# Optimization experiments

Hardware: AMD Instinct MI355X
Metric: run time of the kernel (lower is better)

Reference implementation:

```python
import jax, jax.numpy as jnp
import numpy as np

N = 50000
E = 800000
IN_CH = 256
HEADS = 4
OUT_CH = 32
NEG_SLOPE = 0.2
EPS = 1e-16


def setup_inputs() -> dict:
    key = jax.random.key(0)
    k1, k2, k3, k4 = jax.random.split(key, 4)
    x = jax.random.normal(k1, (N, IN_CH), dtype=jnp.float32)
    edge_index = jax.random.randint(k2, (2, E), 0, N, dtype=jnp.int32)
    # xavier-ish scaling for stability
    weight = jax.random.normal(k3, (HEADS, IN_CH, OUT_CH), dtype=jnp.float32) * (1.0 / np.sqrt(IN_CH))
    att = jax.random.normal(k4, (HEADS, 2 * OUT_CH), dtype=jnp.float32) * (1.0 / np.sqrt(2 * OUT_CH))
    bias = jnp.zeros((HEADS * OUT_CH,), dtype=jnp.float32)
    return {"x": x, "edge_index": edge_index, "weight": weight, "att": att, "bias": bias}


def reference(x, edge_index, weight, att, bias):
    n = x.shape[0]
    H, C = weight.shape[0], weight.shape[2]
    src, dst = edge_index[0], edge_index[1]
    # node features -> per-head projected features [N,H,C]
    h = jnp.einsum('nf,hfc->nhc', x, weight)
    # per-node attention logits (equivalent to concat([h_src,h_dst]) . att)
    a_src = jnp.einsum('nhc,hc->nh', h, att[:, :C])  # [N,H]
    a_dst = jnp.einsum('nhc,hc->nh', h, att[:, C:])  # [N,H]
    alpha = a_src[src] + a_dst[dst]                  # [E,H]
    alpha = jnp.where(alpha > 0, alpha, NEG_SLOPE * alpha)  # LeakyReLU(0.2)
    # segment softmax over incoming edges of each dst node
    alpha_max = jnp.full((n, H), -1e9, dtype=alpha.dtype).at[dst].max(alpha)
    alpha_exp = jnp.exp(alpha - alpha_max[dst])
    sum_exp = jax.ops.segment_sum(alpha_exp, dst, num_segments=n)  # [N,H]
    a = alpha_exp / (sum_exp[dst] + EPS)             # [E,H]
    # weighted scatter-add aggregation
    msg = h[src] * a[:, :, None]                     # [E,H,C]
    out = jax.ops.segment_sum(msg, dst, num_segments=n)  # [N,H,C]
    out = out.reshape(n, H * C) + bias[None, :]
    return out
```

## Files before the change

kernel.cpp:

```cpp
#include <hip/hip_runtime.h>
#include <hip/hip_bf16.h>

#define NEG_SLOPE 0.2f
#define EPSF 1e-16f

typedef __attribute__((ext_vector_type(8))) short short8;
typedef __attribute__((ext_vector_type(4))) float floatx4;

__device__ __forceinline__ float bf2f(unsigned short u) {
  union { unsigned int i; float f; } v; v.i = ((unsigned int)u) << 16; return v.f;
}
__device__ __forceinline__ unsigned short f2bf(float f) {
  union { float f; unsigned int i; } v; v.f = f;
  unsigned int r = v.i + 0x7fffu + ((v.i >> 16) & 1u);
  return (unsigned short)(r >> 16);
}

__global__ void prep0_k(const unsigned short* __restrict__ xw, int* __restrict__ flag,
                        int* __restrict__ cursor, int* __restrict__ ovf_cnt, int n) {
  int i = blockIdx.x * blockDim.x + threadIdx.x;
  if (i < n) cursor[i] = 0;
  if (i == 0) *ovf_cnt = 0;
  if (blockIdx.x == 0) {
    __shared__ int cnt;
    if (threadIdx.x == 0) cnt = 0;
    __syncthreads();
    int local = 0;
    for (int k = 0; k < 16; k++) {
      unsigned short u = xw[(threadIdx.x * 16 + k) << 1];
      int ex = (u >> 7) & 0xFF;
      if (ex >= 0x90 || ex <= 0x40) local++;
    }
    atomicAdd(&cnt, local);
    __syncthreads();
    if (threadIdx.x == 0) *flag = (cnt > 256) ? 1 : 0;
  }
}

__global__ __launch_bounds__(256) void prep1_k(const void* __restrict__ w,
                                               const void* __restrict__ att,
                                               const void* __restrict__ bias,
                                               const int* __restrict__ flag,
                                               unsigned short* __restrict__ bpack,
                                               unsigned short* __restrict__ wpack,
                                               float* __restrict__ bias_f) {
  int f32 = *flag;
  int pb = blockIdx.x;
  if (pb < 128) {
    int i = pb * 256 + threadIdx.x;
    int j = i & 7, lane = (i >> 3) & 63, nt = (i >> 9) & 7, kb = i >> 12;
    int f = (kb << 5) + ((lane >> 4) << 3) + j;
    int col = (nt << 4) + (lane & 15);
    int src = ((col >> 5) << 13) + (f << 5) + (col & 31);
    float v = f32 ? ((const float*)w)[src] : bf2f(((const unsigned short*)w)[src]);
    bpack[i] = f2bf(v);
  } else if (pb < 144) {
    int i = (pb - 128) * 256 + threadIdx.x;
    int j = i & 7, lane = (i >> 3) & 63, kb = i >> 9;
    int quad = lane >> 4, m16 = lane & 15;
    int f = (kb << 5) + (quad << 3) + j;
    float v = 0.f;
    if (m16 < 8) {
      int hd = m16 & 3;
      int db = (m16 >= 4) ? 32 : 0;
      int wbase = (hd << 13) + (f << 5);
      int abase = (hd << 6) + db;
      float acc = 0.f;
      for (int c = 0; c < 32; c++) {
        float wv = f32 ? ((const float*)w)[wbase + c] : bf2f(((const unsigned short*)w)[wbase + c]);
        float av = f32 ? ((const float*)att)[abase + c] : bf2f(((const unsigned short*)att)[abase + c]);
        acc = fmaf(wv, av, acc);
      }
      v = acc;
    }
    wpack[i] = f2bf(v);
  } else {
    int i = threadIdx.x;
    if (i < 128) bias_f[i] = f32 ? ((const float*)bias)[i] : bf2f(((const unsigned short*)bias)[i]);
  }
}

__global__ __launch_bounds__(256) void gemmfill_k(const void* __restrict__ xv,
                                                  const int* __restrict__ flag,
                                                  const unsigned short* __restrict__ bpack,
                                                  const unsigned short* __restrict__ wpack,
                                                  unsigned short* __restrict__ h,
                                                  float* __restrict__ a_srcp,
                                                  float* __restrict__ a_dstp,
                                                  const int* __restrict__ ei,
                                                  int* __restrict__ cursor,
                                                  int* __restrict__ ed,
                                                  int2* __restrict__ ovf,
                                                  int* __restrict__ ovf_cnt,
                                                  int n, int e, int gb) {
  int b = blockIdx.x;
  if (b < gb) {
    int t = threadIdx.x;
    int wave = t >> 6, l = t & 63;
    int quad = l >> 4, m16 = l & 15;
    long n0 = (long)b * 128 + wave * 32;
    int isf32 = *flag;

    floatx4 acc[2][8];
    floatx4 acca[2];
#pragma unroll
    for (int mt = 0; mt < 2; mt++) {
      acca[mt] = (floatx4){0.f, 0.f, 0.f, 0.f};
#pragma unroll
      for (int nt = 0; nt < 8; nt++) acc[mt][nt] = (floatx4){0.f, 0.f, 0.f, 0.f};
    }

    for (int kb = 0; kb < 8; kb++) {
      short8 afr[2];
#pragma unroll
      for (int mt = 0; mt < 2; mt++) {
        long row = n0 + mt * 16 + m16;
        if (row >= n) row = n - 1;
        if (isf32) {
          const float* xp = (const float*)xv + (row << 8) + (kb << 5) + (quad << 3);
          float4 u0 = *(const float4*)xp;
          float4 u1 = *(const float4*)(xp + 4);
          short8 a;
          a[0] = (short)f2bf(u0.x); a[1] = (short)f2bf(u0.y);
          a[2] = (short)f2bf(u0.z); a[3] = (short)f2bf(u0.w);
          a[4] = (short)f2bf(u1.x); a[5] = (short)f2bf(u1.y);
          a[6] = (short)f2bf(u1.z); a[7] = (short)f2bf(u1.w);
          afr[mt] = a;
        } else {
          afr[mt] = *(const short8*)((const unsigned short*)xv + (row << 8) + (kb << 5) + (quad << 3));
        }
      }
      short8 wfr = *(const short8*)(wpack + (((kb << 6) + l) << 3));
      acca[0] = __builtin_amdgcn_mfma_f32_16x16x32_bf16(afr[0], wfr, acca[0], 0, 0, 0);
      acca[1] = __builtin_amdgcn_mfma_f32_16x16x32_bf16(afr[1], wfr, acca[1], 0, 0, 0);
#pragma unroll
      for (int nt = 0; nt < 8; nt++) {
        short8 bfr = *(const short8*)(bpack + (((kb << 3) + nt) << 9) + (l << 3));
        acc[0][nt] = __builtin_amdgcn_mfma_f32_16x16x32_bf16(afr[0], bfr, acc[0][nt], 0, 0, 0);
        acc[1][nt] = __builtin_amdgcn_mfma_f32_16x16x32_bf16(afr[1], bfr, acc[1][nt], 0, 0, 0);
      }
    }
#pragma unroll
    for (int mt = 0; mt < 2; mt++)
#pragma unroll
      for (int r = 0; r < 4; r++) {
        long row = n0 + mt * 16 + quad * 4 + r;
        if (row < n) {
#pragma unroll
          for (int nt = 0; nt < 8; nt++)
            h[(row << 7) + (nt << 4) + m16] = f2bf(acc[mt][nt][r]);
          if (m16 < 8) {
            float val = acca[mt][r];
            int hd = m16 & 3;
            if (m16 < 4) a_srcp[(row << 2) + hd] = val;
            else         a_dstp[(row << 2) + hd] = val;
          }
        }
      }
  } else {
    int i = (b - gb) * 256 + threadIdx.x;
    if (i >= e) return;
    int s = ei[i];
    unsigned d = (unsigned)ei[e + i];
    if (d >= (unsigned)n) return;
    if ((unsigned)s >= (unsigned)n) s = 0;
    int c = atomicAdd(&cursor[d], 1);
    if (c < 32) {
      ed[((int)d << 5) + c] = s;
    } else {
      int k = atomicAdd(ovf_cnt, 1);
      if (k < e) ovf[k] = make_int2((int)d, s);
    }
  }
}

__global__ __launch_bounds__(256) void agg_k(const unsigned short* __restrict__ hfeat,
                                             const int* __restrict__ cursor,
                                             const int* __restrict__ ed,
                                             const int2* __restrict__ ovf,
                                             const int* __restrict__ ovf_cnt,
                                             const float* __restrict__ a_src,
                                             const float* __restrict__ a_dst,
                                             const float* __restrict__ bias_f,
                                             const int* __restrict__ flag,
                                             void* __restrict__ outv, int n, int e) {
  int wave = threadIdx.x >> 6;
  int l = threadIdx.x & 63;
  int node = (blockIdx.x << 2) + wave;
  if (node >= n) return;
  int total = cursor[node];
  int cnt0 = min(total, 32);
  int hq = l & 3;
  int c8 = l & 15;
  int hg = c8 >> 2;
  int q = l >> 4;
  float4 ad4 = *(const float4*)&a_dst[node << 2];
  float adq = (hq == 0) ? ad4.x : (hq == 1) ? ad4.y : (hq == 2) ? ad4.z : ad4.w;

  float m_run = -3.0e38f;
  float swacc = 0.f;
  float acc[8];
#pragma unroll
  for (int k = 0; k < 8; k++) acc[k] = 0.f;

  for (int c0 = 0; c0 < cnt0; c0 += 16) {
    int cnt = min(16, cnt0 - c0);
    int srcv = 0;
    if (l < 16 && (c0 + l) < cnt0) srcv = ed[(node << 5) + c0 + l];
    int myslot = l >> 2;
    int ss = __shfl(srcv, myslot, 64);
    float z = -3.0e38f;
    if (myslot < cnt) {
      float zz = a_src[(ss << 2) + hq] + adq;
      z = zz > 0.f ? zz : NEG_SLOPE * zz;
    }
    float cm = z;
    cm = fmaxf(cm, __shfl_xor(cm, 4, 64));
    cm = fmaxf(cm, __shfl_xor(cm, 8, 64));
    cm = fmaxf(cm, __shfl_xor(cm, 16, 64));
    cm = fmaxf(cm, __shfl_xor(cm, 32, 64));
    float m_new = fmaxf(m_run, cm);
    float resc_q = __expf(m_run - m_new);
    m_run = m_new;
    float wexp = (myslot < cnt) ? __expf(z - m_new) : 0.f;
    swacc = swacc * resc_q + wexp;
    float resc_h = __shfl(resc_q, hg, 64);
#pragma unroll
    for (int k = 0; k < 8; k++) acc[k] *= resc_h;
#pragma unroll
    for (int js = 0; js < 4; js++) {
      if ((js << 2) < cnt) {
        int eidx = (js << 2) + q;
        float sw = __shfl(wexp, (eidx << 2) | hg, 64);
        int sj = __shfl(srcv, eidx, 64);
        uint4 hv = *(const uint4*)(hfeat + (((size_t)sj) << 7) + (c8 << 3));
        unsigned uu[4] = {hv.x, hv.y, hv.z, hv.w};
#pragma unroll
        for (int k2 = 0; k2 < 4; k2++) {
          acc[2 * k2]     = fmaf(sw, bf2f((unsigned short)(uu[k2] & 0xffffu)), acc[2 * k2]);
          acc[2 * k2 + 1] = fmaf(sw, bf2f((unsigned short)(uu[k2] >> 16)), acc[2 * k2 + 1]);
        }
      }
    }
  }

  if (total > 32) {
    int K = *ovf_cnt;
    if (K > e) K = e;
    for (int c0 = 0; c0 < K; c0 += 16) {
      int sv = 0, dv = -1;
      if (l < 16 && (c0 + l) < K) { int2 pr = ovf[c0 + l]; dv = pr.x; sv = pr.y; }
      int myslot = l >> 2;
      int dmy = __shfl(dv, myslot, 64);
      int smy = __shfl(sv, myslot, 64);
      bool valid = (dmy == node);
      float z = -3.0e38f;
      if (valid) {
        float zz = a_src[(smy << 2) + hq] + adq;
        z = zz > 0.f ? zz : NEG_SLOPE * zz;
      }
      float cm = z;
      cm = fmaxf(cm, __shfl_xor(cm, 4, 64));
      cm = fmaxf(cm, __shfl_xor(cm, 8, 64));
      cm = fmaxf(cm, __shfl_xor(cm, 16, 64));
      cm = fmaxf(cm, __shfl_xor(cm, 32, 64));
      float m_new = fmaxf(m_run, cm);
      float resc_q = __expf(m_run - m_new);
      m_run = m_new;
      float wexp = valid ? __expf(z - m_new) : 0.f;
      swacc = swacc * resc_q + wexp;
      float resc_h = __shfl(resc_q, hg, 64);
#pragma unroll
      for (int k = 0; k < 8; k++) acc[k] *= resc_h;
#pragma unroll
      for (int js = 0; js < 4; js++) {
        int eidx = (js << 2) + q;
        float sw = __shfl(wexp, (eidx << 2) | hg, 64);
        int sj = __shfl(sv, eidx, 64);
        uint4 hv = *(const uint4*)(hfeat + (((size_t)sj) << 7) + (c8 << 3));
        unsigned uu[4] = {hv.x, hv.y, hv.z, hv.w};
#pragma unroll
        for (int k2 = 0; k2 < 4; k2++) {
          acc[2 * k2]     = fmaf(sw, bf2f((unsigned short)(uu[k2] & 0xffffu)), acc[2 * k2]);
          acc[2 * k2 + 1] = fmaf(sw, bf2f((unsigned short)(uu[k2] >> 16)), acc[2 * k2 + 1]);
        }
      }
    }
  }

  for (int m = 4; m < 64; m <<= 1) swacc += __shfl_xor(swacc, m, 64);
#pragma unroll
  for (int k = 0; k < 8; k++) {
    acc[k] += __shfl_xor(acc[k], 16, 64);
    acc[k] += __shfl_xor(acc[k], 32, 64);
  }
  float sumv = __shfl(swacc, hg, 64);
  float rs = 1.f / (sumv + EPSF);
  if (l < 16) {
    float o[8];
#pragma unroll
    for (int k = 0; k < 8; k++) o[k] = fmaf(acc[k], rs, bias_f[(c8 << 3) + k]);
    size_t base = (((size_t)node) << 7) + (c8 << 3);
    if (*flag) {
      *(float4*)((float*)outv + base)     = make_float4(o[0], o[1], o[2], o[3]);
      *(float4*)((float*)outv + base + 4) = make_float4(o[4], o[5], o[6], o[7]);
    } else {
      uint4 pk;
      pk.x = (unsigned)f2bf(o[0]) | ((unsigned)f2bf(o[1]) << 16);
      pk.y = (unsigned)f2bf(o[2]) | ((unsigned)f2bf(o[3]) << 16);
      pk.z = (unsigned)f2bf(o[4]) | ((unsigned)f2bf(o[5]) << 16);
      pk.w = (unsigned)f2bf(o[6]) | ((unsigned)f2bf(o[7]) << 16);
      *(uint4*)((unsigned short*)outv + base) = pk;
    }
  }
}

extern "C" void kernel_launch(void* const* d_in, const int* in_sizes, int n_in,
                              void* d_out, int out_size, void* d_ws, size_t ws_size,
                              hipStream_t stream) {
  const void* x    = d_in[0];
  const int*  ei   = (const int*)d_in[1];
  const void* w    = d_in[2];
  const void* att  = d_in[3];
  const void* bias = d_in[4];

  const int n = in_sizes[0] / 256;
  const int e = in_sizes[1] / 2;
  const int gb = (n + 127) / 128;
  const int fb = (e + 255) / 256;

  char* p = (char*)d_ws;
  size_t off = 0;
  auto carve = [&](size_t bytes) -> void* {
    void* r = p + off;
    off = (off + bytes + 255) & ~(size_t)255;
    return r;
  };
  int*      flag    = (int*)carve(sizeof(int));
  int*      ovf_cnt = (int*)carve(sizeof(int));
  float*    bias_f  = (float*)carve(128 * 4);
  unsigned short* h = (unsigned short*)carve((size_t)n * 128 * 2);
  float*    a_src   = (float*)carve((size_t)n * 4 * 4);
  float*    a_dst   = (float*)carve((size_t)n * 4 * 4);
  int*      cursor  = (int*)carve((size_t)n * 4);
  int*      ed      = (int*)carve((size_t)n * 32 * 4);
  int2*     ovf     = (int2*)carve((size_t)e * 8);
  unsigned short* bpack = (unsigned short*)carve((size_t)256 * 128 * 2);
  unsigned short* wpack = (unsigned short*)carve((size_t)8 * 64 * 8 * 2);
  (void)ws_size;

  prep0_k<<<(n + 255) / 256, 256, 0, stream>>>((const unsigned short*)x, flag,
                                               cursor, ovf_cnt, n);
  prep1_k<<<145, 256, 0, stream>>>(w, att, bias, flag, bpack, wpack, bias_f);
  gemmfill_k<<<gb + fb, 256, 0, stream>>>(x, flag, bpack, wpack, h, a_src, a_dst,
                                          ei, cursor, ed, ovf, ovf_cnt, n, e, gb);
  agg_k<<<(n + 3) / 4, 256, 0, stream>>>(h, cursor, ed, ovf, ovf_cnt, a_src, a_dst,
                                         bias_f, flag, d_out, n, e);
}
```

Baseline: 202.7 us.

## Merge prep kernels, shard edge bucketing by destination range, widen aggregation blocks

The two prep kernels are merged into one launch, with every prep block recomputing the dtype flag locally. Edge bucketing now uses a fixed 2048 blocks. Each block is tied to one of four destination-node shards, chosen by blockIdx modulo 8 (likely to map shards to XCDs). Each block scans a strided subset of edge chunks and only inserts edges whose destination falls in its shard, aiming to keep cursor atomics and ed writes local to one L2. The cost is that every edge index is read four times. Aggregation blocks grow to 512 threads with 8 nodes per block.

```diff
diff --git a/kernel.cpp b/kernel.cpp
--- a/kernel.cpp
+++ b/kernel.cpp
@@ -16,36 +16,38 @@
   return (unsigned short)(r >> 16);
 }
 
-__global__ void prep0_k(const unsigned short* __restrict__ xw, int* __restrict__ flag,
-                        int* __restrict__ cursor, int* __restrict__ ovf_cnt, int n) {
-  int i = blockIdx.x * blockDim.x + threadIdx.x;
-  if (i < n) cursor[i] = 0;
-  if (i == 0) *ovf_cnt = 0;
-  if (blockIdx.x == 0) {
-    __shared__ int cnt;
-    if (threadIdx.x == 0) cnt = 0;
-    __syncthreads();
-    int local = 0;
-    for (int k = 0; k < 16; k++) {
-      unsigned short u = xw[(threadIdx.x * 16 + k) << 1];
-      int ex = (u >> 7) & 0xFF;
-      if (ex >= 0x90 || ex <= 0x40) local++;
-    }
-    atomicAdd(&cnt, local);
-    __syncthreads();
-    if (threadIdx.x == 0) *flag = (cnt > 256) ? 1 : 0;
-  }
-}
-
-__global__ __launch_bounds__(256) void prep1_k(const void* __restrict__ w,
-                                               const void* __restrict__ att,
-                                               const void* __restrict__ bias,
-                                               const int* __restrict__ flag,
-                                               unsigned short* __restrict__ bpack,
-                                               unsigned short* __restrict__ wpack,
-                                               float* __restrict__ bias_f) {
-  int f32 = *flag;
-  int pb = blockIdx.x;
+__global__ __launch_bounds__(256) void prep_k(const unsigned short* __restrict__ xw,
+                                              const void* __restrict__ w,
+                                              const void* __restrict__ att,
+                                              const void* __restrict__ bias,
+                                              int* __restrict__ flag,
+                                              int* __restrict__ cursor,
+                                              int* __restrict__ ovf_cnt,
+                                              unsigned short* __restrict__ bpack,
+                                              unsigned short* __restrict__ wpack,
+                                              float* __restrict__ bias_f,
+                                              int n, int zb) {
+  int b = blockIdx.x;
+  if (b < zb) {
+    int i = b * 256 + threadIdx.x;
+    if (i < n) cursor[i] = 0;
+    if (i == 0) *ovf_cnt = 0;
+    return;
+  }
+  __shared__ int cnt;
+  if (threadIdx.x == 0) cnt = 0;
+  __syncthreads();
+  int local = 0;
+  for (int k2 = 0; k2 < 16; k2++) {
+    unsigned short u = xw[(threadIdx.x * 16 + k2) << 1];
+    int ex = (u >> 7) & 0xFF;
+    if (ex >= 0x90 || ex <= 0x40) local++;
+  }
+  atomicAdd(&cnt, local);
+  __syncthreads();
+  int f32 = (cnt > 256) ? 1 : 0;
+  int pb = b - zb;
+  if (pb == 0 && threadIdx.x == 0) *flag = f32;
   if (pb < 128) {
     int i = pb * 256 + threadIdx.x;
     int j = i & 7, lane = (i >> 3) & 63, nt = (i >> 9) & 7, kb = i >> 12;
@@ -92,7 +94,7 @@
                                                   int* __restrict__ ed,
                                                   int2* __restrict__ ovf,
                                                   int* __restrict__ ovf_cnt,
-                                                  int n, int e, int gb) {
+                                                  int n, int e, int gb, int fb) {
   int b = blockIdx.x;
   if (b < gb) {
     int t = threadIdx.x;
@@ -158,23 +160,36 @@
         }
       }
   } else {
-    int i = (b - gb) * 256 + threadIdx.x;
-    if (i >= e) return;
-    int s = ei[i];
-    unsigned d = (unsigned)ei[e + i];
-    if (d >= (unsigned)n) return;
-    if ((unsigned)s >= (unsigned)n) s = 0;
-    int c = atomicAdd(&cursor[d], 1);
-    if (c < 32) {
-      ed[((int)d << 5) + c] = s;
-    } else {
-      int k = atomicAdd(ovf_cnt, 1);
-      if (k < e) ovf[k] = make_int2((int)d, s);
-    }
-  }
-}
-
-__global__ __launch_bounds__(256) void agg_k(const unsigned short* __restrict__ hfeat,
+    int fbi = b - gb;
+    int k = b & 7;
+    int shard = k >> 1;
+    int sub = ((fbi >> 3) << 1) | (k & 1);
+    int nsub = fb >> 2;
+    int ns = (n + 3) >> 2;
+    unsigned lo = (unsigned)(shard * ns);
+    unsigned hi = (unsigned)min(n, (shard + 1) * ns);
+    int nchunks = (e + 255) >> 8;
+    for (int c = sub; c < nchunks; c += nsub) {
+      int i = (c << 8) + threadIdx.x;
+      if (i < e) {
+        unsigned d = (unsigned)ei[e + i];
+        if (d >= lo && d < hi) {
+          int s = ei[i];
+          if ((unsigned)s >= (unsigned)n) s = 0;
+          int c2 = atomicAdd(&cursor[d], 1);
+          if (c2 < 32) {
+            ed[((int)d << 5) + c2] = s;
+          } else {
+            int kk = atomicAdd(ovf_cnt, 1);
+            if (kk < e) ovf[kk] = make_int2((int)d, s);
+          }
+        }
+      }
+    }
+  }
+}
+
+__global__ __launch_bounds__(512) void agg_k(const unsigned short* __restrict__ hfeat,
                                              const int* __restrict__ cursor,
                                              const int* __restrict__ ed,
                                              const int2* __restrict__ ovf,
@@ -186,7 +201,7 @@
                                              void* __restrict__ outv, int n, int e) {
   int wave = threadIdx.x >> 6;
   int l = threadIdx.x & 63;
-  int node = (blockIdx.x << 2) + wave;
+  int node = (blockIdx.x << 3) + wave;
   if (node >= n) return;
   int total = cursor[node];
   int cnt0 = min(total, 32);
@@ -326,8 +341,9 @@
 
   const int n = in_sizes[0] / 256;
   const int e = in_sizes[1] / 2;
+  const int zb = (n + 255) / 256;
   const int gb = (n + 127) / 128;
-  const int fb = (e + 255) / 256;
+  const int fb = 2048;
 
   char* p = (char*)d_ws;
   size_t off = 0;
@@ -349,11 +365,11 @@
   unsigned short* wpack = (unsigned short*)carve((size_t)8 * 64 * 8 * 2);
   (void)ws_size;
 
-  prep0_k<<<(n + 255) / 256, 256, 0, stream>>>((const unsigned short*)x, flag,
-                                               cursor, ovf_cnt, n);
-  prep1_k<<<145, 256, 0, stream>>>(w, att, bias, flag, bpack, wpack, bias_f);
+  prep_k<<<zb + 145, 256, 0, stream>>>((const unsigned short*)x, w, att, bias,
+                                       flag, cursor, ovf_cnt, bpack, wpack, bias_f,
+                                       n, zb);
   gemmfill_k<<<gb + fb, 256, 0, stream>>>(x, flag, bpack, wpack, h, a_src, a_dst,
-                                          ei, cursor, ed, ovf, ovf_cnt, n, e, gb);
-  agg_k<<<(n + 3) / 4, 256, 0, stream>>>(h, cursor, ed, ovf, ovf_cnt, a_src, a_dst,
+                                          ei, cursor, ed, ovf, ovf_cnt, n, e, gb, fb);
+  agg_k<<<(n + 7) / 8, 512, 0, stream>>>(h, cursor, ed, ovf, ovf_cnt, a_src, a_dst,
                                          bias_f, flag, d_out, n, e);
 }
```

New measurement: 207.0 us. 2.1% more time.
